# Kernel optimization log

Hardware: AMD Instinct MI355X
Metric: run time of the kernel (lower is better)

## Reference

```python
import jax, jax.numpy as jnp
import numpy as np


def setup_inputs() -> dict:
    key = jax.random.key(0)
    B, N, C = 16, 4096, 768  # SAM ViT-B token tensor [batch, tokens, channels]
    x = jax.random.normal(key, (B, N, C), dtype=jnp.float32)
    k = 384        # int(C * p2) with p2 = 0.5
    largest = 1    # torch.topk largest=True
    return {"x": x, "k": k, "largest": largest}


def reference(x, k, largest):
    # torch.topk(x, k, dim=2, largest=largest) with dim=2 == last axis for 3D x,
    # then scatter values back into zeros_like(x) at the selected indices.
    if largest:
        vals, idx = jax.lax.top_k(x, k)            # [B, N, k]
    else:
        neg_vals, idx = jax.lax.top_k(-x, k)
        vals = -neg_vals
    B, N, _ = x.shape
    b = jnp.arange(B)[:, None, None]               # broadcast batch index
    n = jnp.arange(N)[None, :, None]               # broadcast token index
    out = jnp.zeros_like(x).at[b, n, idx].set(vals)
    return out
```

## Files before the change

### kernel.cpp

```cpp
#include <hip/hip_runtime.h>
#include <cstdint>


constexpr int C    = 768;
constexpr int TPB  = 256;
constexpr int WPB  = TPB / 64;
constexpr int EPL  = C / 64;
constexpr int NV   = EPL / 4;

__device__ __forceinline__ uint32_t f2key(float f, uint32_t flip) {
    uint32_t b = __float_as_uint(f);
    uint32_t u = (b & 0x80000000u) ? ~b : (b | 0x80000000u);
    return u ^ flip;
}

__global__ __launch_bounds__(TPB) void topk_scatter_row(
        const float* __restrict__ x,
        const int*   __restrict__ pk,
        const int*   __restrict__ plg,
        float*       __restrict__ out,
        int rows) {
    __shared__ int hist_all[WPB][256];

    const int lane = threadIdx.x & 63;
    const int wid  = threadIdx.x >> 6;
    const int row  = blockIdx.x * WPB + wid;
    if (row >= rows) return;

    int* hist = hist_all[wid];

    const float* xr   = x   + (size_t)row * C;
    float*       orow = out + (size_t)row * C;

    const int      k    = pk[0];
    const uint32_t flip = (plg[0] != 0) ? 0u : 0xFFFFFFFFu;

    float    v[EPL];
    uint32_t key[EPL];
    #pragma unroll
    for (int j = 0; j < NV; ++j) {
        float4 t = ((const float4*)xr)[j * 64 + lane];
        v[j*4+0] = t.x; v[j*4+1] = t.y; v[j*4+2] = t.z; v[j*4+3] = t.w;
    }
    #pragma unroll
    for (int e = 0; e < EPL; ++e) key[e] = f2key(v[e], flip);

    if (k <= 0) {
        #pragma unroll
        for (int j = 0; j < NV; ++j)
            ((float4*)orow)[j * 64 + lane] = make_float4(0.f, 0.f, 0.f, 0.f);
        return;
    }

    uint32_t prefix = 0;
    int      kk     = k;
    int      shift  = 24;
    bool     need_tie = false;

    for (int r = 0; r < 4; ++r) {
        ((int4*)hist)[lane] = make_int4(0, 0, 0, 0);

        const uint32_t pmask = (r == 0) ? 0u : ~((1u << (shift + 8)) - 1u);
        #pragma unroll
        for (int e = 0; e < EPL; ++e) {
            if (((key[e] ^ prefix) & pmask) == 0)
                atomicAdd(&hist[(key[e] >> shift) & 255u], 1);
        }

        int4 b = ((const int4*)hist)[lane];
        int t0 = b.x + b.y + b.z + b.w;

        int s = t0;
        #pragma unroll
        for (int off = 1; off < 64; off <<= 1) {
            int o = __shfl_down(s, off);
            s += (lane + off < 64) ? o : 0;
        }
        const int upper = s - t0;

        int ge[4];
        ge[3] = upper + b.w;
        ge[2] = ge[3] + b.z;
        ge[1] = ge[2] + b.y;
        ge[0] = ge[1] + b.x;
        const int bins[4] = { b.x, b.y, b.z, b.w };

        int found_d = -1, found_gt = 0, found_bc = 0;
        #pragma unroll
        for (int i = 0; i < 4; ++i) {
            int gt = ge[i] - bins[i];
            if (gt < kk && kk <= ge[i]) {
                found_d = lane * 4 + i; found_gt = gt; found_bc = bins[i];
            }
        }
        unsigned long long m = __ballot(found_d >= 0);
        int src = __ffsll((long long)m) - 1;
        int d  = __shfl(found_d, src);
        int gt = __shfl(found_gt, src);
        int bc = __shfl(found_bc, src);

        kk -= gt;
        prefix |= ((uint32_t)d) << shift;

        if (kk == bc) break;
        if (shift == 0) { need_tie = true; break; }
        shift -= 8;
    }

    uint32_t selmask = 0;
    if (need_tie) {
        int base = 0;
        #pragma unroll
        for (int j = 0; j < NV; ++j) {
            int eq[4], le = 0;
            #pragma unroll
            for (int c = 0; c < 4; ++c) { eq[c] = (key[j*4+c] == prefix) ? 1 : 0; le += eq[c]; }
            int p = le;
            #pragma unroll
            for (int off = 1; off < 64; off <<= 1) {
                int o = __shfl_up(p, off);
                p += (lane >= off) ? o : 0;
            }
            const int excl = p - le;
            const int tot  = __shfl(p, 63);
            int acc = base + excl;
            #pragma unroll
            for (int c = 0; c < 4; ++c) {
                if (eq[c] && acc < kk) selmask |= 1u << (j*4+c);
                acc += eq[c];
            }
            base += tot;
        }
    }

    #pragma unroll
    for (int j = 0; j < NV; ++j) {
        float4 o;
        float* oo = (float*)&o;
        #pragma unroll
        for (int c = 0; c < 4; ++c) {
            const int e = j*4 + c;
            bool sel = need_tie ? ((key[e] > prefix) || ((selmask >> e) & 1u))
                                : (key[e] >= prefix);
            oo[c] = sel ? v[e] : 0.0f;
        }
        ((float4*)orow)[j * 64 + lane] = o;
    }
}

extern "C" void kernel_launch(void* const* d_in, const int* in_sizes, int n_in,
                              void* d_out, int out_size, void* d_ws, size_t ws_size,
                              hipStream_t stream) {
    const float* x   = (const float*)d_in[0];
    const int*   pk  = (const int*)d_in[1];
    const int*   plg = (const int*)d_in[2];
    float*       out = (float*)d_out;

    const int rows   = in_sizes[0] / C;
    const int blocks = (rows + WPB - 1) / WPB;
    topk_scatter_row<<<blocks, TPB, 0, stream>>>(x, pk, plg, out, rows);
}
```

Measured before the change: 340.4 us.

## Replace LDS radix-histogram top-k select with ballot-based bitwise threshold search

Result: faster. 333.3 us (-2.1%).

```diff
diff --git a/kernel.cpp b/kernel.cpp
--- a/kernel.cpp
+++ b/kernel.cpp
@@ -2,32 +2,32 @@
 #include <cstdint>
 
 
-constexpr int C    = 768;
-constexpr int TPB  = 256;
-constexpr int WPB  = TPB / 64;
-constexpr int EPL  = C / 64;
-constexpr int NV   = EPL / 4;
+constexpr int C   = 768;
+constexpr int TPB = 256;
+constexpr int WPB = TPB / 64;
+constexpr int EPL = C / 64;
+constexpr int NV  = EPL / 4;
 
-__device__ __forceinline__ uint32_t f2key(float f, uint32_t flip) {
-    uint32_t b = __float_as_uint(f);
-    uint32_t u = (b & 0x80000000u) ? ~b : (b | 0x80000000u);
-    return u ^ flip;
+__device__ __forceinline__ uint32_t f2key(uint32_t b, uint32_t flip) {
+    uint32_t m = (uint32_t)((int32_t)b >> 31) | 0x80000000u;
+    return (b ^ m) ^ flip;
+}
+__device__ __forceinline__ float key2f(uint32_t key, uint32_t flip) {
+    uint32_t u = key ^ flip;
+    uint32_t m = (~(uint32_t)((int32_t)u >> 31)) | 0x80000000u;
+    return __uint_as_float(u ^ m);
 }
 
-__global__ __launch_bounds__(TPB) void topk_scatter_row(
+__global__ __launch_bounds__(TPB, 8) void topk_scatter_row(
         const float* __restrict__ x,
         const int*   __restrict__ pk,
         const int*   __restrict__ plg,
         float*       __restrict__ out,
         int rows) {
-    __shared__ int hist_all[WPB][256];
-
     const int lane = threadIdx.x & 63;
     const int wid  = threadIdx.x >> 6;
     const int row  = blockIdx.x * WPB + wid;
     if (row >= rows) return;
-
-    int* hist = hist_all[wid];
 
     const float* xr   = x   + (size_t)row * C;
     float*       orow = out + (size_t)row * C;
@@ -35,15 +35,15 @@
     const int      k    = pk[0];
     const uint32_t flip = (plg[0] != 0) ? 0u : 0xFFFFFFFFu;
 
-    float    v[EPL];
     uint32_t key[EPL];
     #pragma unroll
     for (int j = 0; j < NV; ++j) {
-        float4 t = ((const float4*)xr)[j * 64 + lane];
-        v[j*4+0] = t.x; v[j*4+1] = t.y; v[j*4+2] = t.z; v[j*4+3] = t.w;
+        uint4 t = ((const uint4*)xr)[j * 64 + lane];
+        key[j*4+0] = f2key(t.x, flip);
+        key[j*4+1] = f2key(t.y, flip);
+        key[j*4+2] = f2key(t.z, flip);
+        key[j*4+3] = f2key(t.w, flip);
     }
-    #pragma unroll
-    for (int e = 0; e < EPL; ++e) key[e] = f2key(v[e], flip);
 
     if (k <= 0) {
         #pragma unroll
@@ -51,98 +51,76 @@
             ((float4*)orow)[j * 64 + lane] = make_float4(0.f, 0.f, 0.f, 0.f);
         return;
     }
+    if (k >= C) {
+        #pragma unroll
+        for (int j = 0; j < NV; ++j) {
+            float4 o; float* oo = (float*)&o;
+            #pragma unroll
+            for (int c2 = 0; c2 < 4; ++c2) oo[c2] = key2f(key[j*4+c2], flip);
+            ((float4*)orow)[j * 64 + lane] = o;
+        }
+        return;
+    }
 
-    uint32_t prefix = 0;
-    int      kk     = k;
-    int      shift  = 24;
-    bool     need_tie = false;
-
-    for (int r = 0; r < 4; ++r) {
-        ((int4*)hist)[lane] = make_int4(0, 0, 0, 0);
-
-        const uint32_t pmask = (r == 0) ? 0u : ~((1u << (shift + 8)) - 1u);
+    uint32_t T = 0;
+    bool exact = false;
+    for (int b = 31; b >= 0; --b) {
+        const uint32_t cand = T | (1u << b);
+        int cnt = 0;
         #pragma unroll
-        for (int e = 0; e < EPL; ++e) {
-            if (((key[e] ^ prefix) & pmask) == 0)
-                atomicAdd(&hist[(key[e] >> shift) & 255u], 1);
+        for (int e = 0; e < EPL; ++e)
+            cnt += __popcll(__ballot(key[e] >= cand));
+        if (cnt >= k) {
+            T = cand;
+            if (cnt == k) { exact = true; break; }
         }
-
-        int4 b = ((const int4*)hist)[lane];
-        int t0 = b.x + b.y + b.z + b.w;
-
-        int s = t0;
-        #pragma unroll
-        for (int off = 1; off < 64; off <<= 1) {
-            int o = __shfl_down(s, off);
-            s += (lane + off < 64) ? o : 0;
-        }
-        const int upper = s - t0;
-
-        int ge[4];
-        ge[3] = upper + b.w;
-        ge[2] = ge[3] + b.z;
-        ge[1] = ge[2] + b.y;
-        ge[0] = ge[1] + b.x;
-        const int bins[4] = { b.x, b.y, b.z, b.w };
-
-        int found_d = -1, found_gt = 0, found_bc = 0;
-        #pragma unroll
-        for (int i = 0; i < 4; ++i) {
-            int gt = ge[i] - bins[i];
-            if (gt < kk && kk <= ge[i]) {
-                found_d = lane * 4 + i; found_gt = gt; found_bc = bins[i];
-            }
-        }
-        unsigned long long m = __ballot(found_d >= 0);
-        int src = __ffsll((long long)m) - 1;
-        int d  = __shfl(found_d, src);
-        int gt = __shfl(found_gt, src);
-        int bc = __shfl(found_bc, src);
-
-        kk -= gt;
-        prefix |= ((uint32_t)d) << shift;
-
-        if (kk == bc) break;
-        if (shift == 0) { need_tie = true; break; }
-        shift -= 8;
     }
 
     uint32_t selmask = 0;
-    if (need_tie) {
+    if (exact) {
+        #pragma unroll
+        for (int e = 0; e < EPL; ++e)
+            if (key[e] >= T) selmask |= 1u << e;
+    } else {
+        int cgt = 0;
+        #pragma unroll
+        for (int e = 0; e < EPL; ++e) {
+            if (key[e] > T) selmask |= 1u << e;
+            cgt += __popcll(__ballot(key[e] > T));
+        }
+        const int need = k - cgt;
+        const unsigned long long below = (1ull << lane) - 1ull;
         int base = 0;
         #pragma unroll
         for (int j = 0; j < NV; ++j) {
-            int eq[4], le = 0;
+            int eq[4]; unsigned long long m[4];
             #pragma unroll
-            for (int c = 0; c < 4; ++c) { eq[c] = (key[j*4+c] == prefix) ? 1 : 0; le += eq[c]; }
-            int p = le;
+            for (int c2 = 0; c2 < 4; ++c2) {
+                eq[c2] = (key[j*4+c2] == T) ? 1 : 0;
+                m[c2]  = __ballot(eq[c2] != 0);
+            }
+            int lanebelow = 0;
             #pragma unroll
-            for (int off = 1; off < 64; off <<= 1) {
-                int o = __shfl_up(p, off);
-                p += (lane >= off) ? o : 0;
+            for (int c2 = 0; c2 < 4; ++c2) lanebelow += __popcll(m[c2] & below);
+            int own = 0;
+            #pragma unroll
+            for (int c2 = 0; c2 < 4; ++c2) {
+                if (eq[c2] && (base + lanebelow + own) < need)
+                    selmask |= 1u << (j*4 + c2);
+                own += eq[c2];
             }
-            const int excl = p - le;
-            const int tot  = __shfl(p, 63);
-            int acc = base + excl;
             #pragma unroll
-            for (int c = 0; c < 4; ++c) {
-                if (eq[c] && acc < kk) selmask |= 1u << (j*4+c);
-                acc += eq[c];
-            }
-            base += tot;
+            for (int c2 = 0; c2 < 4; ++c2) base += __popcll(m[c2]);
         }
     }
 
     #pragma unroll
     for (int j = 0; j < NV; ++j) {
-        float4 o;
-        float* oo = (float*)&o;
+        float4 o; float* oo = (float*)&o;
         #pragma unroll
-        for (int c = 0; c < 4; ++c) {
-            const int e = j*4 + c;
-            bool sel = need_tie ? ((key[e] > prefix) || ((selmask >> e) & 1u))
-                                : (key[e] >= prefix);
-            oo[c] = sel ? v[e] : 0.0f;
+        for (int c2 = 0; c2 < 4; ++c2) {
+            const int e = j*4 + c2;
+            oo[c2] = ((selmask >> e) & 1u) ? key2f(key[e], flip) : 0.0f;
         }
         ((float4*)orow)[j * 64 + lane] = o;
     }
```
